# Kernel tuning notes

Measured on AMD Instinct MI355X. Metric: run time of the kernel, lower is better.

The kernel has to match this reference:

```python
import jax, jax.numpy as jnp
import numpy as np
import math

SCALE = 16.0
IGNORE_THRES = 0.5
BAD_CONF_WEIGHT = 1.25
NB, NT, NA, NH, NW, NC = 16, 50, 5, 128, 128, 20


def _inv_tanh(y):
    ys = jnp.clip(y, -1.0 + 1e-6, 1.0 - 1e-6)
    at = 0.5 * jnp.log((1.0 + ys) / (1.0 - ys))
    return jnp.where(y <= -1.0, -2.0, jnp.where(y >= 1.0, 2.0, at))


def _forward(prediction, target, target_sizes, anchors):
    nB, nA, nH, nW, _ = prediction.shape
    nC = prediction.shape[-1] - 6
    s = SCALE
    # scaled anchors and anchor corner points (matches __init__ precompute)
    aw = anchors[:, 0] / s
    ah = anchors[:, 1] / s
    ar = anchors[:, 2]
    cr, sr = jnp.cos(ar), jnp.sin(ar)
    anchor_points = jnp.stack([-cr * aw, sr * aw, cr * aw, -sr * aw,
                               -sr * ah, -cr * ah, sr * ah, cr * ah], axis=1)  # [nA,8]
    anchor_hws = (ah + aw) / 2.0

    pred_conf = prediction[..., 0]
    x = prediction[..., 1]; y = prediction[..., 2]; r = prediction[..., 3]
    h = prediction[..., 4]; w = prediction[..., 5]
    pred_cls = prediction[..., 6:]

    # ---- build_targets_dist, vectorized (original uses detached .cpu().data) ----
    tgt = jax.lax.stop_gradient(target)
    T = tgt.shape[1]
    valid = jnp.arange(T)[None, :] < target_sizes[:, None]
    gx = tgt[..., 0] / s; gy = tgt[..., 1] / s
    gw = tgt[..., 4] / s; gh = tgt[..., 3] / s
    gr = tgt[..., 2]
    valid = valid & (gw != 0) & (gh != 0)
    gi = jnp.clip(gx.astype(jnp.int32), 0, nW - 1)
    gj = jnp.clip(gy.astype(jnp.int32), 0, nH - 1)
    pts = tgt[..., 5:13] / s
    cpts = pts - jnp.tile(jnp.stack([gx, gy], axis=-1), (1, 1, 4))  # centered corners [nB,T,8]
    deltas = cpts[:, :, None, :] - anchor_points[None, None, :, :]  # [nB,T,nA,8]
    dn = sum(jnp.linalg.norm(deltas[..., i:i + 2], axis=-1) for i in (0, 2, 4, 6))
    norm = (((gh + gw) / 2.0)[:, :, None] + anchor_hws[None, None, :]) / 2.0
    anch_dists = (dn / norm) ** 2  # [nB,T,nA]

    # conf_mask: zero anchors closer than ignore_thres at (gj,gi)
    conf_mask = jnp.ones((nB, nA, nH, nW), jnp.float32)
    b3 = jnp.broadcast_to(jnp.arange(nB)[:, None, None], (nB, T, nA)).reshape(-1)
    a3 = jnp.broadcast_to(jnp.arange(nA)[None, None, :], (nB, T, nA)).reshape(-1)
    gj3 = jnp.broadcast_to(gj[:, :, None], (nB, T, nA)).reshape(-1)
    gi3 = jnp.broadcast_to(gi[:, :, None], (nB, T, nA)).reshape(-1)
    ign = ((anch_dists < IGNORE_THRES) & valid[:, :, None]).reshape(-1)
    conf_mask = conf_mask.at[b3, a3, gj3, gi3].min(jnp.where(ign, 0.0, 1.0))

    best_n = jnp.argmin(anch_dists, axis=-1)  # [nB,T]
    txv = _inv_tanh(gx - (gi.astype(jnp.float32) + 0.5))
    tyv = _inv_tanh(gy - (gj.astype(jnp.float32) + 0.5))
    rd = gr - ar[best_n]
    rd = jnp.where(rd > math.pi, rd - 2 * math.pi,
                   jnp.where(rd < -math.pi, rd + 2 * math.pi, rd))
    trv = _inv_tanh(rd / (math.pi / 2))
    twv = jnp.log(gw / aw[best_n] + 1e-16)
    thv = jnp.log(gh / ah[best_n] + 1e-16)
    tlabv = jnp.argmax(tgt[..., 13:], axis=-1)

    bS = jnp.where(valid, jnp.arange(nB)[:, None], -1).reshape(-1)  # -1 -> dropped
    idx = (bS, best_n.reshape(-1), gj.reshape(-1), gi.reshape(-1))
    z = jnp.zeros((nB, nA, nH, nW), jnp.float32)
    mask = z.at[idx].set(1.0, mode='drop')
    conf_mask = conf_mask.at[idx].set(1.0, mode='drop')
    tx = z.at[idx].set(txv.reshape(-1), mode='drop')
    ty = z.at[idx].set(tyv.reshape(-1), mode='drop')
    tw = z.at[idx].set(twv.reshape(-1), mode='drop')
    th = z.at[idx].set(thv.reshape(-1), mode='drop')
    tr = z.at[idx].set(trv.reshape(-1), mode='drop')
    tconf = mask  # tconf set to 1 exactly where mask is 1
    tlab = jnp.zeros((nB, nA, nH, nW), jnp.int32).at[idx].set(
        tlabv.reshape(-1).astype(jnp.int32), mode='drop')

    conf_mask_false = conf_mask * (1.0 - mask)

    def masked_bce(z_, t_, m_):
        l = jnp.maximum(z_, 0.0) - z_ * t_ + jnp.log1p(jnp.exp(-jnp.abs(z_)))
        return jnp.sum(l * m_) / jnp.maximum(jnp.sum(m_), 1.0)

    def masked_mse(p_, t_):
        return jnp.sum(((p_ - t_) ** 2) * mask) / jnp.maximum(jnp.sum(mask), 1.0)

    loss_conf = BAD_CONF_WEIGHT * masked_bce(pred_conf, tconf, conf_mask_false) \
        + masked_bce(pred_conf, tconf, mask)
    loss_x = masked_mse(x, tx); loss_y = masked_mse(y, ty)
    loss_w = masked_mse(w, tw); loss_h = masked_mse(h, th)
    loss_r = masked_mse(r, tr)
    logp = jax.nn.log_softmax(pred_cls, axis=-1)
    nll = -jnp.take_along_axis(logp, tlab[..., None], axis=-1)[..., 0]
    loss_cls = jnp.sum(nll * mask) / jnp.maximum(jnp.sum(mask), 1.0)
    return loss_x + loss_y + loss_w + loss_h + loss_r + loss_conf + loss_cls


def setup_inputs():
    key = jax.random.key(0)
    ks = jax.random.split(key, 8)
    s = SCALE
    prediction = jax.random.normal(ks[0], (NB, NA, NH, NW, 6 + NC), jnp.float32) * 0.5
    # targets in image pixel space (grid is NHxNW at stride SCALE)
    cx = jax.random.uniform(ks[1], (NB, NT), minval=1.0, maxval=NW - 1.0) * s
    cy = jax.random.uniform(ks[2], (NB, NT), minval=1.0, maxval=NH - 1.0) * s
    bw = jax.random.uniform(ks[3], (NB, NT), minval=8.0, maxval=96.0)
    bh = jax.random.uniform(ks[4], (NB, NT), minval=8.0, maxval=48.0)
    br = jax.random.uniform(ks[5], (NB, NT), minval=-0.3, maxval=0.3)
    c, si = jnp.cos(br), jnp.sin(br)
    pts = jnp.stack([cx - c * bw, cy + si * bw, cx + c * bw, cy - si * bw,
                     cx - si * bh, cy - c * bh, cx + si * bh, cy + c * bh], axis=-1)
    cls = jax.nn.one_hot(jax.random.randint(ks[6], (NB, NT), 0, NC), NC, dtype=jnp.float32)
    target = jnp.concatenate([jnp.stack([cx, cy, br, bh, bw], axis=-1), pts, cls], axis=-1)
    target_sizes = jax.random.randint(ks[7], (NB,), 20, NT + 1).astype(jnp.int32)
    anchors = jnp.array([[48., 16., 0.], [96., 24., 0.], [192., 32., 0.],
                         [64., 64., 0.], [32., 96., 1.5708]], jnp.float32)
    return {"prediction": prediction, "target": target,
            "target_sizes": target_sizes, "anchors": anchors}


def reference(prediction, target, target_sizes, anchors):
    return _forward(prediction, target, target_sizes, anchors)
```

## Files before the change

### kernel.cpp

```cpp
#include <hip/hip_runtime.h>
#include <math.h>

#define NBb 16
#define NTt 50
#define NAa 5
#define NHh 128
#define NWw 128
#define NCc 20
#define NCH 26
#define NCELL (NBb*NAa*NHh*NWw)
#define NREC  (NBb*NTt)
#define SCALE_F 16.0f
#define IGNORE_THRES_F 0.5f
#define BAD_CONF_WEIGHT_F 1.25f
#define PI_F 3.14159265358979323846f

#define STATUS_OFF_F 16
#define REC_OFF_F (16 + NCELL)

__device__ __forceinline__ float inv_tanh_f(float y) {
  if (y <= -1.0f) return -2.0f;
  if (y >= 1.0f)  return  2.0f;
  float ys = fminf(fmaxf(y, -1.0f + 1e-6f), 1.0f - 1e-6f);
  return 0.5f * logf((1.0f + ys) / (1.0f - ys));
}

__device__ __forceinline__ float softplus_f(float z) {
  return fmaxf(z, 0.0f) + log1pf(expf(-fabsf(z)));
}

__global__ void k_prep(const float* __restrict__ tgt,
                       const int* __restrict__ tsz,
                       const float* __restrict__ anch,
                       float* __restrict__ ws) {
  int tid = blockIdx.x * blockDim.x + threadIdx.x;
  if (tid >= NREC) return;
  int b = tid / NTt, t = tid % NTt;

  float aw[NAa], ah[NAa], ar[NAa], ahw[NAa], ap[NAa][8];
  for (int a = 0; a < NAa; ++a) {
    aw[a] = anch[a*3+0] / SCALE_F;
    ah[a] = anch[a*3+1] / SCALE_F;
    ar[a] = anch[a*3+2];
    float cr = cosf(ar[a]), sr = sinf(ar[a]);
    ap[a][0] = -cr*aw[a]; ap[a][1] =  sr*aw[a];
    ap[a][2] =  cr*aw[a]; ap[a][3] = -sr*aw[a];
    ap[a][4] = -sr*ah[a]; ap[a][5] = -cr*ah[a];
    ap[a][6] =  sr*ah[a]; ap[a][7] =  cr*ah[a];
    ahw[a] = (ah[a] + aw[a]) * 0.5f;
  }

  const float* row = tgt + (size_t)tid * (13 + NCc);
  float gx = row[0] / SCALE_F;
  float gy = row[1] / SCALE_F;
  float gr = row[2];
  float gh = row[3] / SCALE_F;
  float gw = row[4] / SCALE_F;
  bool valid = (t < tsz[b]) && (gw != 0.0f) && (gh != 0.0f);
  if (!valid) return;

  int gi = (int)gx; gi = min(max(gi, 0), NWw - 1);
  int gj = (int)gy; gj = min(max(gj, 0), NHh - 1);

  float cp[8];
  for (int k = 0; k < 8; ++k)
    cp[k] = row[5 + k] / SCALE_F - ((k & 1) ? gy : gx);

  float bestd = 1e30f; int best = 0; unsigned ignm = 0;
  for (int a = 0; a < NAa; ++a) {
    float dn = 0.0f;
    for (int p = 0; p < 8; p += 2) {
      float dx = cp[p]   - ap[a][p];
      float dy = cp[p+1] - ap[a][p+1];
      dn += sqrtf(dx*dx + dy*dy);
    }
    float nm = ((gh + gw) * 0.5f + ahw[a]) * 0.5f;
    float d = dn / nm; d = d * d;
    if (d < IGNORE_THRES_F) ignm |= (1u << a);
    if (d < bestd) { bestd = d; best = a; }
  }

  unsigned* status = (unsigned*)(ws + STATUS_OFF_F);
  int cellbase = ((b * NAa) * NHh + gj) * NWw + gi;
  for (int a = 0; a < NAa; ++a)
    if ((ignm >> a) & 1u) atomicMax(&status[cellbase + a * NHh * NWw], 1u);
  atomicMax(&status[cellbase + best * NHh * NWw], 2u + (unsigned)tid);

  float txv = inv_tanh_f(gx - ((float)gi + 0.5f));
  float tyv = inv_tanh_f(gy - ((float)gj + 0.5f));
  float rd = gr - ar[best];
  if (rd > PI_F) rd -= 2.0f * PI_F;
  else if (rd < -PI_F) rd += 2.0f * PI_F;
  float trv = inv_tanh_f(rd / (PI_F * 0.5f));
  float twv = logf(gw / aw[best] + 1e-16f);
  float thv = logf(gh / ah[best] + 1e-16f);
  int tlab = 0; float bm = row[13];
  for (int c = 1; c < NCc; ++c)
    if (row[13 + c] > bm) { bm = row[13 + c]; tlab = c; }

  float* rec = ws + REC_OFF_F;
  rec[0*NREC + tid] = txv;
  rec[1*NREC + tid] = tyv;
  rec[2*NREC + tid] = twv;
  rec[3*NREC + tid] = thv;
  rec[4*NREC + tid] = trv;
  ((int*)rec)[5*NREC + tid] = tlab;
}

__global__ void k_main(const float* __restrict__ pred, float* __restrict__ ws) {
  const unsigned* __restrict__ status = (const unsigned*)(ws + STATUS_OFF_F);
  const float* __restrict__ rec = ws + REC_OFF_F;
  float acc_bg = 0.0f, cnt_bg = 0.0f;
  int stride = gridDim.x * blockDim.x;
  for (int i = blockIdx.x * blockDim.x + threadIdx.x; i < NCELL; i += stride) {
    unsigned st = status[i];
    const float* cell = pred + (size_t)i * NCH;
    if (st == 0u) {
      acc_bg += softplus_f(cell[0]);
      cnt_bg += 1.0f;
    } else if (st >= 2u) {
      int r = (int)(st - 2u);
      float z = cell[0];
      float lobj = softplus_f(z) - z;
      float dx = cell[1] - rec[0*NREC + r];
      float dy = cell[2] - rec[1*NREC + r];
      float dr = cell[3] - rec[4*NREC + r];
      float dh = cell[4] - rec[3*NREC + r];
      float dw = cell[5] - rec[2*NREC + r];
      int tlab = ((const int*)rec)[5*NREC + r];
      float m = cell[6];
      for (int c = 1; c < NCc; ++c) m = fmaxf(m, cell[6 + c]);
      float s = 0.0f;
      for (int c = 0; c < NCc; ++c) s += expf(cell[6 + c] - m);
      float nll = (m + logf(s)) - cell[6 + tlab];
      atomicAdd(ws + 2, lobj);
      atomicAdd(ws + 3, dx * dx);
      atomicAdd(ws + 4, dy * dy);
      atomicAdd(ws + 5, dw * dw);
      atomicAdd(ws + 6, dh * dh);
      atomicAdd(ws + 7, dr * dr);
      atomicAdd(ws + 8, nll);
      atomicAdd(ws + 9, 1.0f);
    }
  }
  for (int off = 32; off; off >>= 1) {
    acc_bg += __shfl_down(acc_bg, off, 64);
    cnt_bg += __shfl_down(cnt_bg, off, 64);
  }
  __shared__ float s0[8], s1[8];
  int wid = threadIdx.x >> 6, lane = threadIdx.x & 63;
  if (lane == 0) { s0[wid] = acc_bg; s1[wid] = cnt_bg; }
  __syncthreads();
  if (threadIdx.x == 0) {
    float a = 0.0f, c = 0.0f;
    int nw = blockDim.x >> 6;
    for (int w = 0; w < nw; ++w) { a += s0[w]; c += s1[w]; }
    atomicAdd(ws + 0, a);
    atomicAdd(ws + 1, c);
  }
}

__global__ void k_final(const float* __restrict__ ws, float* __restrict__ out) {
  float acc_bg = ws[0], cnt_bg = ws[1], acc_obj = ws[2];
  float ax = ws[3], ay = ws[4], aww = ws[5], ahh = ws[6], arr = ws[7], acls = ws[8];
  float cm = ws[9];
  float db = fmaxf(cnt_bg, 1.0f);
  float dm = fmaxf(cm, 1.0f);
  float loss_conf = BAD_CONF_WEIGHT_F * (acc_bg / db) + acc_obj / dm;
  out[0] = (ax + ay + aww + ahh + arr + acls) / dm + loss_conf;
}

extern "C" void kernel_launch(void* const* d_in, const int* in_sizes, int n_in,
                              void* d_out, int out_size, void* d_ws, size_t ws_size,
                              hipStream_t stream) {
  const float* pred = (const float*)d_in[0];
  const float* tgt  = (const float*)d_in[1];
  const int*   tsz  = (const int*)d_in[2];
  const float* anch = (const float*)d_in[3];
  float* ws = (float*)d_ws;

  hipMemsetAsync(d_ws, 0, (size_t)(STATUS_OFF_F + NCELL) * sizeof(float), stream);
  k_prep<<<4, 256, 0, stream>>>(tgt, tsz, anch, ws);
  k_main<<<1280, 256, 0, stream>>>(pred, ws);
  k_final<<<1, 1, 0, stream>>>(ws, (float*)d_out);
}
```

Before: 258.2 us.

## Sum softplus over all cells with float4 reads, subtract non-background cells

Background loss now comes from a softplus sum over every cell's confidence. A new kernel streams the prediction tensor as float4 and picks out the confidence channel by index arithmetic. A second kernel visits only cells with nonzero status and subtracts their softplus and count through atomics. This removes the strided 26-float gather per cell, but it reads the whole tensor, about 26x more bytes than the confidence channel alone, and does global atomics per marked cell.

```diff
diff --git a/kernel.cpp b/kernel.cpp
--- a/kernel.cpp
+++ b/kernel.cpp
@@ -9,6 +9,8 @@
 #define NCc 20
 #define NCH 26
 #define NCELL (NBb*NAa*NHh*NWw)
+#define NFLAT (NCELL*NCH)
+#define NQ4   (NFLAT/4)
 #define NREC  (NBb*NTt)
 #define SCALE_F 16.0f
 #define IGNORE_THRES_F 0.5f
@@ -107,20 +109,43 @@
   ((int*)rec)[5*NREC + tid] = tlab;
 }
 
-__global__ void k_main(const float* __restrict__ pred, float* __restrict__ ws) {
+__global__ void k_sum(const float4* __restrict__ pred4, float* __restrict__ ws) {
+  float acc = 0.0f;
+  int stride = gridDim.x * blockDim.x;
+  for (int q = blockIdx.x * blockDim.x + threadIdx.x; q < NQ4; q += stride) {
+    float4 v = pred4[q];
+    int r = (q * 4) % 26;
+    if (r == 0)       acc += softplus_f(v.x);
+    else if (r == 25) acc += softplus_f(v.y);
+    else if (r == 24) acc += softplus_f(v.z);
+    else if (r == 23) acc += softplus_f(v.w);
+  }
+  for (int off = 32; off; off >>= 1) acc += __shfl_down(acc, off, 64);
+  __shared__ float s0[8];
+  int wid = threadIdx.x >> 6, lane = threadIdx.x & 63;
+  if (lane == 0) s0[wid] = acc;
+  __syncthreads();
+  if (threadIdx.x == 0) {
+    float a = 0.0f;
+    int nw = blockDim.x >> 6;
+    for (int w = 0; w < nw; ++w) a += s0[w];
+    atomicAdd(ws + 0, a);
+  }
+}
+
+__global__ void k_fix(const float* __restrict__ pred, float* __restrict__ ws) {
   const unsigned* __restrict__ status = (const unsigned*)(ws + STATUS_OFF_F);
   const float* __restrict__ rec = ws + REC_OFF_F;
-  float acc_bg = 0.0f, cnt_bg = 0.0f;
   int stride = gridDim.x * blockDim.x;
   for (int i = blockIdx.x * blockDim.x + threadIdx.x; i < NCELL; i += stride) {
     unsigned st = status[i];
+    if (st == 0u) continue;
     const float* cell = pred + (size_t)i * NCH;
-    if (st == 0u) {
-      acc_bg += softplus_f(cell[0]);
-      cnt_bg += 1.0f;
-    } else if (st >= 2u) {
+    float z = cell[0];
+    atomicAdd(ws + 10, softplus_f(z));
+    atomicAdd(ws + 11, 1.0f);
+    if (st >= 2u) {
       int r = (int)(st - 2u);
-      float z = cell[0];
       float lobj = softplus_f(z) - z;
       float dx = cell[1] - rec[0*NREC + r];
       float dy = cell[2] - rec[1*NREC + r];
@@ -143,25 +168,12 @@
       atomicAdd(ws + 9, 1.0f);
     }
   }
-  for (int off = 32; off; off >>= 1) {
-    acc_bg += __shfl_down(acc_bg, off, 64);
-    cnt_bg += __shfl_down(cnt_bg, off, 64);
-  }
-  __shared__ float s0[8], s1[8];
-  int wid = threadIdx.x >> 6, lane = threadIdx.x & 63;
-  if (lane == 0) { s0[wid] = acc_bg; s1[wid] = cnt_bg; }
-  __syncthreads();
-  if (threadIdx.x == 0) {
-    float a = 0.0f, c = 0.0f;
-    int nw = blockDim.x >> 6;
-    for (int w = 0; w < nw; ++w) { a += s0[w]; c += s1[w]; }
-    atomicAdd(ws + 0, a);
-    atomicAdd(ws + 1, c);
-  }
 }
 
 __global__ void k_final(const float* __restrict__ ws, float* __restrict__ out) {
-  float acc_bg = ws[0], cnt_bg = ws[1], acc_obj = ws[2];
+  float acc_bg = ws[0] - ws[10];
+  float cnt_bg = (float)NCELL - ws[11];
+  float acc_obj = ws[2];
   float ax = ws[3], ay = ws[4], aww = ws[5], ahh = ws[6], arr = ws[7], acls = ws[8];
   float cm = ws[9];
   float db = fmaxf(cnt_bg, 1.0f);
@@ -181,6 +193,7 @@
 
   hipMemsetAsync(d_ws, 0, (size_t)(STATUS_OFF_F + NCELL) * sizeof(float), stream);
   k_prep<<<4, 256, 0, stream>>>(tgt, tsz, anch, ws);
-  k_main<<<1280, 256, 0, stream>>>(pred, ws);
+  k_sum<<<4096, 256, 0, stream>>>((const float4*)pred, ws);
+  k_fix<<<2048, 256, 0, stream>>>(pred, ws);
   k_final<<<1, 1, 0, stream>>>(ws, (float*)d_out);
 }
```

After: 305.1 us. +18.2%, slower.
